# Performance work log

Hardware: AMD Instinct MI355X
Metric: run time of the kernel (lower is better)

The kernel has to match this reference:

```python
import jax, jax.numpy as jnp
import numpy as np

B, L, A, BD, K, M, FP, R, T = 256, 128, 39, 10, 6, 256, 256, 3, 2


def _gru(x, h, w_ih, w_hh, b_ih, b_hh):
    # PyTorch GRUCell: gates ordered (reset, update, new)
    gi = x @ w_ih.T + b_ih
    gh = h @ w_hh.T + b_hh
    i_r, i_z, i_n = jnp.split(gi, 3, axis=-1)
    h_r, h_z, h_n = jnp.split(gh, 3, axis=-1)
    r = jax.nn.sigmoid(i_r + h_r)
    z = jax.nn.sigmoid(i_z + h_z)
    n = jnp.tanh(i_n + r * h_n)
    return (1.0 - z) * n + z * h


def setup_inputs() -> dict:
    key = jax.random.key(0)
    ks = jax.random.split(key, 26)
    n = lambda i, shape: jax.random.normal(ks[i], shape, jnp.float32) * 0.05
    return dict(
        atom_list=jax.random.normal(ks[0], (B, L, A), jnp.float32),
        bond_list=jax.random.normal(ks[1], (B, M, BD), jnp.float32),
        atom_degree_list=jax.random.randint(ks[2], (B, L, K), 0, L),
        bond_degree_list=jax.random.randint(ks[3], (B, L, K), 0, M),
        atom_mask=jnp.ones((B, L), jnp.float32),
        atom_fc_W=n(4, (FP, A)), atom_fc_b=n(5, (FP,)),
        neighbor_fc_W=n(6, (FP, A + BD)), neighbor_fc_b=n(7, (FP,)),
        gru_w_ih=n(8, (R, 3 * FP, FP)), gru_w_hh=n(9, (R, 3 * FP, FP)),
        gru_b_ih=n(10, (R, 3 * FP)), gru_b_hh=n(11, (R, 3 * FP)),
        align_W=n(12, (R, 1, 2 * FP)), align_b=n(13, (R, 1)),
        attend_W=n(14, (R, FP, FP)), attend_b=n(15, (R, FP)),
        mol_gru_w_ih=n(16, (3 * FP, FP)), mol_gru_w_hh=n(17, (3 * FP, FP)),
        mol_gru_b_ih=n(18, (3 * FP,)), mol_gru_b_hh=n(19, (3 * FP,)),
        mol_align_W=n(20, (1, 2 * FP)), mol_align_b=n(21, (1,)),
        mol_attend_W=n(22, (FP, FP)), mol_attend_b=n(23, (FP,)),
    )


def reference(atom_list, bond_list, atom_degree_list, bond_degree_list, atom_mask,
              atom_fc_W, atom_fc_b, neighbor_fc_W, neighbor_fc_b,
              gru_w_ih, gru_w_hh, gru_b_ih, gru_b_hh,
              align_W, align_b, attend_W, attend_b,
              mol_gru_w_ih, mol_gru_w_hh, mol_gru_b_ih, mol_gru_b_hh,
              mol_align_W, mol_align_b, mol_attend_W, mol_attend_b):
    Bn, Ln, _ = atom_list.shape
    Fp = atom_fc_W.shape[0]
    gather = jax.vmap(lambda t, i: t[i])  # per-batch row gather

    atom_pre = atom_list @ atom_fc_W.T + atom_fc_b          # (B,L,FP) pre-relu
    atom_feature = jax.nn.relu(atom_pre)
    afv = [atom_pre]

    bond_neighbor = gather(bond_list, bond_degree_list)      # (B,L,K,BD)
    atom_neighbor = gather(atom_list, atom_degree_list)      # (B,L,K,A)
    nf = jax.nn.relu(jnp.concatenate([atom_neighbor, bond_neighbor], -1)
                     @ neighbor_fc_W.T + neighbor_fc_b)       # (B,L,K,FP)

    pad = atom_degree_list == Ln - 1                          # padding-atom index
    attend_mask = jnp.where(pad, 0.0, 1.0)[..., None]
    softmax_mask = jnp.where(pad, -9.0, 0.0)[..., None]

    h = atom_feature.reshape(Bn * Ln, Fp)
    act = atom_feature
    awv = []
    for d in range(R):
        neigh = nf if d == 0 else gather(act, atom_degree_list)
        fa = jnp.concatenate(
            [jnp.broadcast_to(act[:, :, None, :], neigh.shape), neigh], -1)
        score = jax.nn.relu(fa @ align_W[d].T + align_b[d]) + softmax_mask
        aw = jax.nn.softmax(score, axis=-2) * attend_mask     # (B,L,K,1)
        awv.append(aw)
        ctx = jax.nn.relu(jnp.sum(aw * (neigh @ attend_W[d].T + attend_b[d]), -2))
        h = _gru(ctx.reshape(Bn * Ln, Fp), h,
                 gru_w_ih[d], gru_w_hh[d], gru_b_ih[d], gru_b_hh[d])
        atom_feature = h.reshape(Bn, Ln, Fp)
        act = jax.nn.relu(atom_feature)
        afv.append(act)

    m3 = atom_mask[..., None]
    mol_unb = [jnp.sum(atom_feature * m3, -2)]
    mol_feature = jnp.sum(act * m3, -2)
    act_mol = jax.nn.relu(mol_feature)
    mfv = [mol_feature]
    mawv = []
    mol_smask = jnp.where(m3 == 0, -9e8, 0.0)
    for _ in range(T):
        ma = jnp.concatenate(
            [jnp.broadcast_to(act_mol[:, None, :], act.shape), act], -1)
        ms = jax.nn.relu(ma @ mol_align_W.T + mol_align_b) + mol_smask
        mw = jax.nn.softmax(ms, axis=-2) * m3                 # (B,L,1)
        mawv.append(mw)
        mctx = jax.nn.relu(jnp.sum(mw * (act @ mol_attend_W.T + mol_attend_b), -2))
        mol_feature = _gru(mctx, mol_feature,
                           mol_gru_w_ih, mol_gru_w_hh, mol_gru_b_ih, mol_gru_b_hh)
        mol_unb.append(mol_feature)
        act_mol = jax.nn.relu(mol_feature)
        mfv.append(act_mol)

    return (atom_feature, jnp.stack(afv), jnp.stack(awv), jnp.stack(mfv),
            jnp.stack(mol_unb), jnp.stack(mawv), mol_feature)
```

## Files before the change

kernel.cpp:

```cpp
#include <hip/hip_runtime.h>
#include <hip/hip_bf16.h>

#define BB 256
#define LL 128
#define AA 39
#define BDD 10
#define KK 6
#define MM 256
#define FP 256
#define RR 3
#define TT 2

using short8  = __attribute__((ext_vector_type(8))) short;
using short4v = __attribute__((ext_vector_type(4))) short;
using f32x4   = __attribute__((ext_vector_type(4))) float;
using f32x2   = __attribute__((ext_vector_type(2))) float;

__device__ __forceinline__ short f2bf(float f) {
    union { float f; unsigned u; } v; v.f = f;
    unsigned u = v.u;
    u += 0x7fffu + ((u >> 16) & 1u);
    return (short)(u >> 16);
}
__device__ __forceinline__ float bf2f(short s) {
    union { unsigned u; float f; } v; v.u = ((unsigned)(unsigned short)s) << 16;
    return v.f;
}
__device__ __forceinline__ float wred64(float v) {
#pragma unroll
    for (int off = 32; off >= 1; off >>= 1) v += __shfl_xor(v, off);
    return v;
}

#define GLL(gp, lp) __builtin_amdgcn_global_load_lds( \
    (const __attribute__((address_space(1))) void*)(gp), \
    (__attribute__((address_space(3))) void*)(lp), 16, 0, 0)

__global__ __launch_bounds__(256) void k_transpose(const float* __restrict__ src,
                                                   float* __restrict__ dst, int O, int I) {
    int idx = blockIdx.x * 256 + threadIdx.x;
    if (idx >= O * I) return;
    int o = idx / I, i = idx - o * I;
    dst[i * O + o] = src[idx];
}

__global__ __launch_bounds__(256) void k_prep_gruw(const float* __restrict__ gwih,
                                                   const float* __restrict__ gwhh,
                                                   short* __restrict__ out) {
    int idx = blockIdx.x * 256 + threadIdx.x;
    if (idx >= RR * 2 * 8 * 48 * 512) return;
    int j = idx & 7;
    int lane = (idx >> 3) & 63;
    int blk = idx >> 9;
    int nt = blk % 48;
    int ks = (blk / 48) % 8;
    int mat = (blk / (48 * 8)) % 2;
    int d = blk / (48 * 8 * 2);
    int n = nt * 16 + (lane & 15);
    int k = ks * 32 + (lane >> 4) * 8 + j;
    const float* W = mat ? gwhh : gwih;
    out[idx] = f2bf(W[((size_t)d * 768 + n) * FP + k]);
}

__global__ __launch_bounds__(256) void k_prep_molfrag(const float* __restrict__ mih,
                                                      const float* __restrict__ mhh,
                                                      short* __restrict__ out) {
    int idx = blockIdx.x * 256 + threadIdx.x;
    if (idx >= 2 * 8 * 48 * 512) return;
    int j = idx & 7;
    int lane = (idx >> 3) & 63;
    int blk = idx >> 9;
    int nt = blk % 48;
    int ks = (blk / 48) % 8;
    int mat = blk / (48 * 8);
    int n = nt * 16 + (lane & 15);
    int k = ks * 32 + (lane >> 4) * 8 + j;
    const float* W = mat ? mhh : mih;
    out[idx] = f2bf(W[(size_t)n * FP + k]);
}

__global__ __launch_bounds__(256) void k_prep_waf(const float* __restrict__ atW,
                                                  short* __restrict__ out) {
    int idx = blockIdx.x * 256 + threadIdx.x;
    if (idx >= RR * 8 * 16 * 512) return;
    int j = idx & 7;
    int lane = (idx >> 3) & 63;
    int blk = idx >> 9;
    int nt = blk % 16;
    int ks = (blk / 16) % 8;
    int d = blk / 128;
    int n = nt * 16 + (lane & 15);
    int k = ks * 32 + (lane >> 4) * 8 + j;
    out[idx] = f2bf(atW[(size_t)d * FP * FP + (size_t)n * FP + k]);
}

__global__ __launch_bounds__(256) void k_atom_pre(const float* __restrict__ atom_list,
                                                  const float* __restrict__ WafcT,
                                                  const float* __restrict__ afc_b,
                                                  const float* __restrict__ WnT,
                                                  const float* __restrict__ bn,
                                                  float* __restrict__ out_pre,
                                                  float* __restrict__ hbuf,
                                                  short* __restrict__ hb16,
                                                  short* __restrict__ ApreB) {
    int g0 = blockIdx.x * 8;
    int t = threadIdx.x;
    __shared__ float x[8][AA];
    for (int i = t; i < 8 * AA; i += 256) x[i / AA][i % AA] = atom_list[(size_t)g0 * AA + i];
    __syncthreads();
    float a1[8], a2[8];
    float b1 = afc_b[t], b2 = bn[t];
#pragma unroll
    for (int a = 0; a < 8; ++a) { a1[a] = b1; a2[a] = b2; }
    for (int i = 0; i < AA; ++i) {
        float w1 = WafcT[i * FP + t];
        float w2 = WnT[i * FP + t];
#pragma unroll
        for (int a = 0; a < 8; ++a) { a1[a] += x[a][i] * w1; a2[a] += x[a][i] * w2; }
    }
#pragma unroll
    for (int a = 0; a < 8; ++a) {
        size_t idx = (size_t)(g0 + a) * FP + t;
        out_pre[idx] = a1[a];
        float rl = fmaxf(a1[a], 0.f);
        hbuf[idx] = rl;
        hb16[idx] = f2bf(rl);
        ApreB[idx] = f2bf(a2[a]);
    }
}

__global__ __launch_bounds__(512) void k_awn_d0(
        const short* __restrict__ ACTB,
        const short* __restrict__ SRC,
        const float* __restrict__ bond_list,
        const int* __restrict__ adeg, const int* __restrict__ bdeg,
        const float* __restrict__ WnT,
        const float* __restrict__ alignW, const float* __restrict__ alignBp,
        short* __restrict__ wn_out, float* __restrict__ sw_out,
        float* __restrict__ awv_out) {
    __shared__ short snb[LL * FP];
    const int b = blockIdx.x >> 1;
    const int half = blockIdx.x & 1;
    const int t = threadIdx.x;
    const int wave = t >> 6, lane = t & 63;

    {
        const char* src = (const char*)(SRC + (size_t)b * LL * FP);
#pragma unroll
        for (int it = 0; it < 8; ++it) {
            int off = it * 8192 + wave * 1024 + lane * 16;
            GLL(src + off, (char*)snb + it * 8192 + wave * 1024);
        }
    }

    f32x4 w0 = *(const f32x4*)(alignW + lane * 4);
    f32x4 w1 = *(const f32x4*)(alignW + FP + lane * 4);
    float bias = alignBp[0];

    float wnt[BDD][4];
#pragma unroll
    for (int i = 0; i < BDD; ++i) {
        f32x4 v = *(const f32x4*)(WnT + (AA + i) * FP + lane * 4);
#pragma unroll
        for (int q = 0; q < 4; ++q) wnt[i][q] = v[q];
    }

    __syncthreads();

#pragma unroll
    for (int ai = 0; ai < 8; ++ai) {
        const int al = half * 64 + wave * 8 + ai;
        const int ga = b * LL + al;

        short4v sv = *(const short4v*)(ACTB + (size_t)ga * FP + lane * 4);
        float ss = wred64(bf2f(sv[0]) * w0[0] + bf2f(sv[1]) * w0[1] +
                          bf2f(sv[2]) * w0[2] + bf2f(sv[3]) * w0[3]);

        int jx[KK];
#pragma unroll
        for (int k = 0; k < KK; ++k) jx[k] = adeg[ga * KK + k];

        float nf[KK][4];
        float sc[KK];
#pragma unroll
        for (int k = 0; k < KK; ++k) {
            short4v nv = *(const short4v*)(snb + jx[k] * FP + lane * 4);
            float f0 = bf2f(nv[0]), f1 = bf2f(nv[1]), f2 = bf2f(nv[2]), f3 = bf2f(nv[3]);
            int bi = bdeg[ga * KK + k];
            const float* bp = bond_list + ((size_t)b * MM + bi) * BDD;
            float bb[BDD];
#pragma unroll
            for (int i = 0; i < 5; ++i) {
                f32x2 v2 = *(const f32x2*)(bp + 2 * i);
                bb[2 * i] = v2[0]; bb[2 * i + 1] = v2[1];
            }
            float b0 = 0.f, b1 = 0.f, b2 = 0.f, b3 = 0.f;
#pragma unroll
            for (int i = 0; i < BDD; ++i) {
                b0 += bb[i] * wnt[i][0]; b1 += bb[i] * wnt[i][1];
                b2 += bb[i] * wnt[i][2]; b3 += bb[i] * wnt[i][3];
            }
            f0 = fmaxf(f0 + b0, 0.f); f1 = fmaxf(f1 + b1, 0.f);
            f2 = fmaxf(f2 + b2, 0.f); f3 = fmaxf(f3 + b3, 0.f);
            nf[k][0] = f0; nf[k][1] = f1; nf[k][2] = f2; nf[k][3] = f3;
            float s2 = wred64(f0 * w1[0] + f1 * w1[1] + f2 * w1[2] + f3 * w1[3]);
            float s = fmaxf(ss + s2 + bias, 0.f);
            if (jx[k] == LL - 1) s -= 9.0f;
            sc[k] = s;
        }

        float m = sc[0];
#pragma unroll
        for (int k = 1; k < KK; ++k) m = fmaxf(m, sc[k]);
        float e[KK], den = 0.f;
#pragma unroll
        for (int k = 0; k < KK; ++k) { e[k] = expf(sc[k] - m); den += e[k]; }
        float aw[KK], sumaw = 0.f;
#pragma unroll
        for (int k = 0; k < KK; ++k) {
            aw[k] = (jx[k] == LL - 1) ? 0.f : e[k] / den;
            sumaw += aw[k];
        }
        if (lane < KK) {
            float av = aw[0];
#pragma unroll
            for (int k = 1; k < KK; ++k) if (lane == k) av = aw[k];
            awv_out[(size_t)ga * KK + lane] = av;
        }
        if (lane == 0) sw_out[ga] = sumaw;

        short4v wo;
#pragma unroll
        for (int q = 0; q < 4; ++q) {
            float w = 0.f;
#pragma unroll
            for (int k = 0; k < KK; ++k) w += aw[k] * nf[k][q];
            wo[q] = f2bf(w);
        }
        *(short4v*)(wn_out + (size_t)ga * FP + lane * 4) = wo;
    }
}

__global__ __launch_bounds__(512) void k_ctx_mfma(
        const short* __restrict__ XB,
        const float* __restrict__ SW,
        const short* __restrict__ WaF,
        const float* __restrict__ ab,
        short* __restrict__ ctx_out) {
    __shared__ short lds[2][8192];
    const int t = threadIdx.x;
    const int wave = t >> 6, lane = t & 63;
    const int abase = blockIdx.x * 32 + (wave >> 2) * 16;
    const int wn4 = wave & 3;
    const int lr = lane & 15, lk = lane >> 4;
    const int kofs = blockIdx.x & 7;

#define CSTAGE(i) do { \
        int ke_ = ((i) + kofs) & 7; \
        _Pragma("unroll") \
        for (int e = 0; e < 2; ++e) { \
            int f = wave * 2 + e; \
            GLL(WaF + (size_t)(ke_ * 16 + f) * 512 + lane * 8, &lds[(i) & 1][f * 512]); \
        } } while (0)

    f32x4 acc[4] = {};
    const short8* xrow = (const short8*)(XB + (size_t)(abase + lr) * FP);

    CSTAGE(0);
#pragma unroll
    for (int i = 0; i < 8; ++i) {
        int ke = (i + kofs) & 7;
        short8 ax = xrow[ke * 4 + lk];
        __syncthreads();
        if (i < 7) CSTAGE(i + 1);
#pragma unroll
        for (int sub = 0; sub < 4; ++sub) {
            int nt = wn4 * 4 + sub;
            short8 bf = *(const short8*)(&lds[i & 1][nt * 512 + lane * 8]);
            acc[sub] = __builtin_amdgcn_mfma_f32_16x16x32_bf16(ax, bf, acc[sub], 0, 0, 0);
        }
    }
#undef CSTAGE

#pragma unroll
    for (int sub = 0; sub < 4; ++sub) {
        int c = wn4 * 64 + sub * 16 + lr;
        float abc = ab[c];
#pragma unroll
        for (int q = 0; q < 4; ++q) {
            int atom = abase + lk * 4 + q;
            float v = acc[sub][q] + SW[atom] * abc;
            ctx_out[(size_t)atom * FP + c] = f2bf(fmaxf(v, 0.f));
        }
    }
}

__global__ __launch_bounds__(512) void k_actx(int d,
        const short* __restrict__ ACTB,
        const int* __restrict__ adeg,
        const float* __restrict__ alW, const float* __restrict__ alb,
        const short* __restrict__ WaF, const float* __restrict__ atb,
        short* __restrict__ ctx_out, float* __restrict__ awv_out) {
    __shared__ __align__(16) short aS[32768];
    __shared__ __align__(16) short cS[32768];
    __shared__ int   jxS[LL * KK];
    __shared__ float awS[LL * KK];
    __shared__ float swS[LL];

    const int b = blockIdx.x;
    const int t = threadIdx.x;
    const int wave = t >> 6, lane = t & 63;
    const int lr = lane & 15, lk = lane >> 4;

#define SLAB_OFF(r, cb) ((((r) * 512 + (cb))) ^ ((((r) & 7)) << 4))
#define A4R(r, c)  (*(const short4v*)((const char*)aS + SLAB_OFF(r, (c) * 2)))
#define C8R(r, c)  (*(const short8*)((const char*)cS + SLAB_OFF(r, (c) * 2)))
#define CW4(r, c, v) (*(short4v*)((char*)cS + SLAB_OFF(r, (c) * 2)) = (v))

    {
        const char* src = (const char*)(ACTB + (size_t)b * LL * FP);
#pragma unroll
        for (int it = 0; it < 8; ++it) {
            int off = it * 8192 + wave * 1024 + lane * 16;
            int so = off ^ (((off >> 9) & 7) << 4);
            GLL(src + so, (char*)aS + off);
        }
        for (int i = t; i < LL * KK; i += 512) jxS[i] = adeg[b * LL * KK + i];
    }
    __syncthreads();

    {
        f32x4 w0 = *(const f32x4*)(alW + (size_t)d * 2 * FP + lane * 4);
        f32x4 w1 = *(const f32x4*)(alW + (size_t)d * 2 * FP + FP + lane * 4);
        float bias = alb[d];
        for (int ai = 0; ai < 16; ++ai) {
            int a = wave * 16 + ai;
            short4v sv = A4R(a, lane * 4);
            float ss = wred64(bf2f(sv[0]) * w0[0] + bf2f(sv[1]) * w0[1] +
                              bf2f(sv[2]) * w0[2] + bf2f(sv[3]) * w0[3]);
            float sc[KK]; int jx[KK];
#pragma unroll
            for (int k = 0; k < KK; ++k) {
                int j = jxS[a * KK + k]; jx[k] = j;
                short4v nv = A4R(j, lane * 4);
                float s2 = wred64(bf2f(nv[0]) * w1[0] + bf2f(nv[1]) * w1[1] +
                                  bf2f(nv[2]) * w1[2] + bf2f(nv[3]) * w1[3]);
                float s = fmaxf(ss + s2 + bias, 0.f);
                if (j == LL - 1) s -= 9.0f;
                sc[k] = s;
            }
            float m = sc[0];
#pragma unroll
            for (int k = 1; k < KK; ++k) m = fmaxf(m, sc[k]);
            float e[KK], den = 0.f;
#pragma unroll
            for (int k = 0; k < KK; ++k) { e[k] = expf(sc[k] - m); den += e[k]; }
            float aw[KK], sumaw = 0.f;
#pragma unroll
            for (int k = 0; k < KK; ++k) {
                aw[k] = (jx[k] == LL - 1) ? 0.f : e[k] / den;
                sumaw += aw[k];
            }
            if (lane < KK) {
                float av = aw[0];
#pragma unroll
                for (int k = 1; k < KK; ++k) if (lane == k) av = aw[k];
                awS[a * KK + lane] = av;
                awv_out[((size_t)b * LL + a) * KK + lane] = av;
            }
            if (lane == 0) swS[a] = sumaw;
        }
    }
    __syncthreads();

    for (int ai = 0; ai < 16; ++ai) {
        int a = wave * 16 + ai;
        float a0 = 0.f, a1 = 0.f, a2 = 0.f, a3 = 0.f;
#pragma unroll
        for (int k = 0; k < KK; ++k) {
            float awv = awS[a * KK + k];
            short4v nv = A4R(jxS[a * KK + k], lane * 4);
            a0 += awv * bf2f(nv[0]);
            a1 += awv * bf2f(nv[1]);
            a2 += awv * bf2f(nv[2]);
            a3 += awv * bf2f(nv[3]);
        }
        short4v wo; wo[0] = f2bf(a0); wo[1] = f2bf(a1); wo[2] = f2bf(a2); wo[3] = f2bf(a3);
        CW4(a, lane * 4, wo);
    }
    __syncthreads();

    {
        const int rg = wave >> 1, csl = wave & 1;
        f32x4 acc[2][8] = {};
        const short8* wb = (const short8*)(WaF + (size_t)d * 8 * 16 * 512);
        for (int ks = 0; ks < 8; ++ks) {
            short8 a0 = C8R(rg * 32 + lr, ks * 32 + lk * 8);
            short8 a1 = C8R(rg * 32 + 16 + lr, ks * 32 + lk * 8);
#pragma unroll
            for (int nt2 = 0; nt2 < 8; ++nt2) {
                short8 bf = wb[(size_t)(ks * 16 + csl * 8 + nt2) * 64 + lane];
                acc[0][nt2] = __builtin_amdgcn_mfma_f32_16x16x32_bf16(a0, bf, acc[0][nt2], 0, 0, 0);
                acc[1][nt2] = __builtin_amdgcn_mfma_f32_16x16x32_bf16(a1, bf, acc[1][nt2], 0, 0, 0);
            }
        }
#pragma unroll
        for (int rt = 0; rt < 2; ++rt)
#pragma unroll
        for (int nt2 = 0; nt2 < 8; ++nt2) {
            int col = csl * 128 + nt2 * 16 + lr;
            float abv = atb[d * FP + col];
#pragma unroll
            for (int q = 0; q < 4; ++q) {
                int row = rg * 32 + rt * 16 + lk * 4 + q;
                float v = acc[rt][nt2][q] + swS[row] * abv;
                ctx_out[((size_t)b * LL + row) * FP + col] = f2bf(fmaxf(v, 0.f));
            }
        }
    }
#undef SLAB_OFF
#undef A4R
#undef C8R
#undef CW4
}

template<int LAST>
__global__ __launch_bounds__(512) void k_gru_mfma(
        const short* __restrict__ XB,
        const short* __restrict__ HBl,
        float* __restrict__ hbuf,
        const short* __restrict__ Bih,
        const short* __restrict__ Bhh,
        const float* __restrict__ bih, const float* __restrict__ bhh,
        float* __restrict__ act_out,
        short* __restrict__ HB_out,
        short* __restrict__ ACT_out) {
    __shared__ short ldsB[3][12288];
    __shared__ short ldsA[2][16384];
    const int t = threadIdx.x;
    const int wave = t >> 6, lane = t & 63;
    const int rh = wave >> 2;
    const int wn = wave & 3;
    const int lr = lane & 15, lk = lane >> 4;
    const int bid = blockIdx.x;
    const int kofs = bid & 7;
    const int abase = bid * 64;

#define PKS(p)  ((((p) >> 2) + kofs) & 7)
#define STAGEP(p) do { \
        const short* base_ = ((((p) >> 1) & 1) ? Bhh : Bih) + (size_t)PKS(p) * 24576; \
        const int h_ = (p) & 1; \
        _Pragma("unroll") \
        for (int e = 0; e < 3; ++e) { \
            int j = wave * 3 + e; \
            int nt = 4 * (j >> 1) + 2 * h_ + (j & 1); \
            GLL(base_ + nt * 512 + lane * 8, &ldsB[(p) % 3][j * 512]); \
        } } while (0)
#define LDA_READ(s, r, c) (*(const short8*)((const char*)ldsA[s] + \
        ((((r) * 512 + (c) * 2)) ^ ((((r) & 7)) << 4))))
#define LDA_READ1(s, r, c) (*(const short*)((const char*)ldsA[s] + \
        ((((r) * 512 + (c) * 2)) ^ ((((r) & 7)) << 4))))

    {
        const char* xsrc = (const char*)(XB + (size_t)abase * FP);
        const char* hsrc = (const char*)(HBl + (size_t)abase * FP);
#pragma unroll
        for (int it = 0; it < 4; ++it) {
            int off = it * 8192 + wave * 1024 + lane * 16;
            int src = off ^ (((off >> 9) & 7) << 4);
            GLL(xsrc + src, (char*)ldsA[0] + off);
            GLL(hsrc + src, (char*)ldsA[1] + off);
        }
    }
    STAGEP(0);
    STAGEP(1);

    f32x4 acc_rz[2][8] = {};
    f32x4 acc_in[2][4] = {};
    f32x4 acc_hn[2][4] = {};

    short8 ax0{}, ah0{}, ax1{}, ah1{};
#pragma unroll
    for (int p = 0; p < 32; ++p) {
        if (p < 31) { asm volatile("s_waitcnt vmcnt(3)" ::: "memory"); }
        else        { asm volatile("s_waitcnt vmcnt(0)" ::: "memory"); }
        __builtin_amdgcn_s_barrier();
        __builtin_amdgcn_sched_barrier(0);
        if (p < 30) STAGEP(p + 2);
        const int h_ = p & 1;
        const int mat = (p >> 1) & 1;
        if ((p & 3) == 0) {
            int ks = PKS(p);
            int c = ks * 32 + lk * 8;
            ax0 = LDA_READ(0, rh * 32 + lr, c);
            ah0 = LDA_READ(1, rh * 32 + lr, c);
            ax1 = LDA_READ(0, rh * 32 + 16 + lr, c);
            ah1 = LDA_READ(1, rh * 32 + 16 + lr, c);
        }
#pragma unroll
        for (int rg = 0; rg < 2; ++rg) {
            const short8 a8 = mat ? (rg ? ah1 : ah0) : (rg ? ax1 : ax0);
#pragma unroll
            for (int g = 0; g < 3; ++g) {
#pragma unroll
                for (int s2 = 0; s2 < 2; ++s2) {
                    const int sub = 2 * h_ + s2;
                    const int j = ((4 * g + wn) << 1) | s2;
                    short8 bf = *(const short8*)(&ldsB[p % 3][j * 512 + lane * 8]);
                    if (g < 2)
                        acc_rz[rg][g * 4 + sub] = __builtin_amdgcn_mfma_f32_16x16x32_bf16(a8, bf, acc_rz[rg][g * 4 + sub], 0, 0, 0);
                    else if (mat)
                        acc_hn[rg][sub] = __builtin_amdgcn_mfma_f32_16x16x32_bf16(a8, bf, acc_hn[rg][sub], 0, 0, 0);
                    else
                        acc_in[rg][sub] = __builtin_amdgcn_mfma_f32_16x16x32_bf16(a8, bf, acc_in[rg][sub], 0, 0, 0);
                }
            }
        }
    }
#undef STAGEP
#undef PKS

#pragma unroll
    for (int sub = 0; sub < 4; ++sub) {
        int c = wn * 64 + sub * 16 + lr;
        float brz_r = bih[c] + bhh[c];
        float brz_z = bih[FP + c] + bhh[FP + c];
        float bin_ = bih[2 * FP + c];
        float bhn = bhh[2 * FP + c];
#pragma unroll
        for (int rg = 0; rg < 2; ++rg) {
#pragma unroll
            for (int q = 0; q < 4; ++q) {
                int row = rh * 32 + rg * 16 + lk * 4 + q;
                int atom = abase + row;
                size_t idx = (size_t)atom * FP + c;
                float hold = bf2f(LDA_READ1(1, row, c));
                float r = 1.f / (1.f + expf(-(acc_rz[rg][0 * 4 + sub][q] + brz_r)));
                float z = 1.f / (1.f + expf(-(acc_rz[rg][1 * 4 + sub][q] + brz_z)));
                float n = tanhf(acc_in[rg][sub][q] + bin_ + r * (acc_hn[rg][sub][q] + bhn));
                float hn = (1.f - z) * n + z * hold;
                float rl = fmaxf(hn, 0.f);
                act_out[idx] = rl;
                if constexpr (LAST) {
                    hbuf[idx] = hn;
                } else {
                    HB_out[idx] = f2bf(hn);
                    ACT_out[idx] = f2bf(rl);
                }
            }
        }
    }
#undef LDA_READ
#undef LDA_READ1
}

__global__ __launch_bounds__(256) void k_mol_reduce(const float* __restrict__ hbuf,
                                                    const float* __restrict__ act,
                                                    const float* __restrict__ mask,
                                                    const float* __restrict__ malW,
                                                    float* __restrict__ o_unb0,
                                                    float* __restrict__ o_mfv0,
                                                    float* __restrict__ molF,
                                                    short* __restrict__ MOLFb,
                                                    float* __restrict__ S2g) {
    int b = blockIdx.x, t = threadIdx.x;
    int wave = t >> 6, lane = t & 63;
    float s1 = 0.f, s2 = 0.f;
    for (int l = 0; l < LL; ++l) {
        float mk = mask[b * LL + l];
        s1 += hbuf[((size_t)b * LL + l) * FP + t] * mk;
        s2 += act[((size_t)b * LL + l) * FP + t] * mk;
    }
    o_unb0[b * FP + t] = s1;
    o_mfv0[b * FP + t] = s2;
    molF[b * FP + t] = s2;
    MOLFb[b * FP + t] = f2bf(s2);

    for (int l = wave; l < LL; l += 4) {
        float v2 = 0.f;
#pragma unroll
        for (int q = 0; q < 4; ++q) {
            int i = lane + 64 * q;
            v2 += act[((size_t)b * LL + l) * FP + i] * malW[FP + i];
        }
        v2 = wred64(v2);
        if (lane == 0) S2g[b * LL + l] = v2;
    }
}

__global__ __launch_bounds__(256) void k_mstep(int step,
        const float* __restrict__ act,
        const float* __restrict__ molF,
        const float* __restrict__ mask,
        const float* __restrict__ S2g,
        const float* __restrict__ malW, const float* __restrict__ malb,
        const float* __restrict__ MWaT, const float* __restrict__ matb,
        short* __restrict__ MCTXb,
        float* __restrict__ o_mawv) {
    int b = blockIdx.x, t = threadIdx.x;
    int wave = t >> 6, lane = t & 63;
    __shared__ float sS[LL], mwS[LL], waS[FP];
    __shared__ float red[4];

    float hprev = molF[b * FP + t];
    float am = fmaxf(hprev, 0.f);

    float v = am * malW[t];
    v = wred64(v);
    if (lane == 0) red[wave] = v;
    __syncthreads();
    float s_self = red[0] + red[1] + red[2] + red[3];

    if (t < LL) {
        float s = fmaxf(s_self + S2g[b * LL + t] + malb[0], 0.f);
        if (mask[b * LL + t] == 0.f) s += -9e8f;
        sS[t] = s;
    }
    __syncthreads();

    float m = -1e30f;
    for (int l = 0; l < LL; ++l) m = fmaxf(m, sS[l]);
    float den = 0.f;
    for (int l = 0; l < LL; ++l) den += expf(sS[l] - m);
    if (t < LL) {
        float w = expf(sS[t] - m) / den * mask[b * LL + t];
        mwS[t] = w;
        o_mawv[(size_t)step * (BB * LL) + b * LL + t] = w;
    }
    __syncthreads();

    float sumaw = 0.f;
    for (int l = 0; l < LL; ++l) sumaw += mwS[l];

    float wa = 0.f;
    for (int l = 0; l < LL; ++l) wa += mwS[l] * act[((size_t)b * LL + l) * FP + t];
    waS[t] = wa;
    __syncthreads();

    float acc = sumaw * matb[t];
    for (int i = 0; i < FP; ++i) acc += waS[i] * MWaT[i * FP + t];
    MCTXb[b * FP + t] = f2bf(fmaxf(acc, 0.f));
}

__global__ __launch_bounds__(512) void k_mol_gru(int step,
        const short* __restrict__ XB,
        const short* __restrict__ HBl,
        const short* __restrict__ Bih,
        const short* __restrict__ Bhh,
        const float* __restrict__ bih, const float* __restrict__ bhh,
        float* __restrict__ o_unb, float* __restrict__ o_mfv,
        float* __restrict__ molF, short* __restrict__ MOLFb,
        float* __restrict__ o_molfeat) {
    __shared__ short ldsB[3][12288];
    __shared__ short ldsA[2][16384];
    const int t = threadIdx.x;
    const int wave = t >> 6, lane = t & 63;
    const int rh = wave >> 2;
    const int wn = wave & 3;
    const int lr = lane & 15, lk = lane >> 4;
    const int bid = blockIdx.x;
    const int kofs = bid & 7;
    const int abase = bid * 64;

#define PKS(p)  ((((p) >> 2) + kofs) & 7)
#define STAGEP(p) do { \
        const short* base_ = ((((p) >> 1) & 1) ? Bhh : Bih) + (size_t)PKS(p) * 24576; \
        const int h_ = (p) & 1; \
        _Pragma("unroll") \
        for (int e = 0; e < 3; ++e) { \
            int j = wave * 3 + e; \
            int nt = 4 * (j >> 1) + 2 * h_ + (j & 1); \
            GLL(base_ + nt * 512 + lane * 8, &ldsB[(p) % 3][j * 512]); \
        } } while (0)
#define LDA_READ(s, r, c) (*(const short8*)((const char*)ldsA[s] + \
        ((((r) * 512 + (c) * 2)) ^ ((((r) & 7)) << 4))))
#define LDA_READ1(s, r, c) (*(const short*)((const char*)ldsA[s] + \
        ((((r) * 512 + (c) * 2)) ^ ((((r) & 7)) << 4))))

    {
        const char* xsrc = (const char*)(XB + (size_t)abase * FP);
        const char* hsrc = (const char*)(HBl + (size_t)abase * FP);
#pragma unroll
        for (int it = 0; it < 4; ++it) {
            int off = it * 8192 + wave * 1024 + lane * 16;
            int src = off ^ (((off >> 9) & 7) << 4);
            GLL(xsrc + src, (char*)ldsA[0] + off);
            GLL(hsrc + src, (char*)ldsA[1] + off);
        }
    }
    STAGEP(0);
    STAGEP(1);

    f32x4 acc_rz[2][8] = {};
    f32x4 acc_in[2][4] = {};
    f32x4 acc_hn[2][4] = {};

    short8 ax0{}, ah0{}, ax1{}, ah1{};
#pragma unroll
    for (int p = 0; p < 32; ++p) {
        if (p < 31) { asm volatile("s_waitcnt vmcnt(3)" ::: "memory"); }
        else        { asm volatile("s_waitcnt vmcnt(0)" ::: "memory"); }
        __builtin_amdgcn_s_barrier();
        __builtin_amdgcn_sched_barrier(0);
        if (p < 30) STAGEP(p + 2);
        const int h_ = p & 1;
        const int mat = (p >> 1) & 1;
        if ((p & 3) == 0) {
            int ks = PKS(p);
            int c = ks * 32 + lk * 8;
            ax0 = LDA_READ(0, rh * 32 + lr, c);
            ah0 = LDA_READ(1, rh * 32 + lr, c);
            ax1 = LDA_READ(0, rh * 32 + 16 + lr, c);
            ah1 = LDA_READ(1, rh * 32 + 16 + lr, c);
        }
#pragma unroll
        for (int rg = 0; rg < 2; ++rg) {
            const short8 a8 = mat ? (rg ? ah1 : ah0) : (rg ? ax1 : ax0);
#pragma unroll
            for (int g = 0; g < 3; ++g) {
#pragma unroll
                for (int s2 = 0; s2 < 2; ++s2) {
                    const int sub = 2 * h_ + s2;
                    const int j = ((4 * g + wn) << 1) | s2;
                    short8 bf = *(const short8*)(&ldsB[p % 3][j * 512 + lane * 8]);
                    if (g < 2)
                        acc_rz[rg][g * 4 + sub] = __builtin_amdgcn_mfma_f32_16x16x32_bf16(a8, bf, acc_rz[rg][g * 4 + sub], 0, 0, 0);
                    else if (mat)
                        acc_hn[rg][sub] = __builtin_amdgcn_mfma_f32_16x16x32_bf16(a8, bf, acc_hn[rg][sub], 0, 0, 0);
                    else
                        acc_in[rg][sub] = __builtin_amdgcn_mfma_f32_16x16x32_bf16(a8, bf, acc_in[rg][sub], 0, 0, 0);
                }
            }
        }
    }
#undef STAGEP
#undef PKS

#pragma unroll
    for (int sub = 0; sub < 4; ++sub) {
        int c = wn * 64 + sub * 16 + lr;
        float brz_r = bih[c] + bhh[c];
        float brz_z = bih[FP + c] + bhh[FP + c];
        float bin_ = bih[2 * FP + c];
        float bhn = bhh[2 * FP + c];
#pragma unroll
        for (int rg = 0; rg < 2; ++rg) {
#pragma unroll
            for (int q = 0; q < 4; ++q) {
                int row = rh * 32 + rg * 16 + lk * 4 + q;
                int m = abase + row;
                size_t idx = (size_t)m * FP + c;
                float hold = bf2f(LDA_READ1(1, row, c));
                float r = 1.f / (1.f + expf(-(acc_rz[rg][0 * 4 + sub][q] + brz_r)));
                float z = 1.f / (1.f + expf(-(acc_rz[rg][1 * 4 + sub][q] + brz_z)));
                float n = tanhf(acc_in[rg][sub][q] + bin_ + r * (acc_hn[rg][sub][q] + bhn));
                float hn = (1.f - z) * n + z * hold;
                o_unb[(size_t)(step + 1) * (BB * FP) + idx] = hn;
                o_mfv[(size_t)(step + 1) * (BB * FP) + idx] = fmaxf(hn, 0.f);
                molF[idx] = hn;
                MOLFb[idx] = f2bf(hn);
                if (step == TT - 1) o_molfeat[idx] = hn;
            }
        }
    }
#undef LDA_READ
#undef LDA_READ1
}

extern "C" void kernel_launch(void* const* d_in, const int* in_sizes, int n_in,
                              void* d_out, int out_size, void* d_ws, size_t ws_size,
                              hipStream_t stream) {
    const float* atom_list = (const float*)d_in[0];
    const float* bond_list = (const float*)d_in[1];
    const int*   adeg      = (const int*)d_in[2];
    const int*   bdeg      = (const int*)d_in[3];
    const float* amask     = (const float*)d_in[4];
    const float* atom_fc_W = (const float*)d_in[5];
    const float* atom_fc_b = (const float*)d_in[6];
    const float* nfc_W     = (const float*)d_in[7];
    const float* nfc_b     = (const float*)d_in[8];
    const float* gwih      = (const float*)d_in[9];
    const float* gwhh      = (const float*)d_in[10];
    const float* gbih      = (const float*)d_in[11];
    const float* gbhh      = (const float*)d_in[12];
    const float* alW       = (const float*)d_in[13];
    const float* alb       = (const float*)d_in[14];
    const float* atW       = (const float*)d_in[15];
    const float* atb       = (const float*)d_in[16];
    const float* mgwih     = (const float*)d_in[17];
    const float* mgwhh     = (const float*)d_in[18];
    const float* mgbih     = (const float*)d_in[19];
    const float* mgbhh     = (const float*)d_in[20];
    const float* malW      = (const float*)d_in[21];
    const float* malb      = (const float*)d_in[22];
    const float* matW      = (const float*)d_in[23];
    const float* matb      = (const float*)d_in[24];

    const size_t BLF = (size_t)BB * LL * FP;
    float* out = (float*)d_out;
    float* O0 = out;
    float* O1 = out + BLF;
    float* O2 = O1 + 4 * BLF;
    float* O3 = O2 + (size_t)RR * BB * LL * KK;
    float* O4 = O3 + (size_t)(TT + 1) * BB * FP;
    float* O5 = O4 + (size_t)(TT + 1) * BB * FP;
    float* O6 = O5 + (size_t)TT * BB * LL;

    float* ws = (float*)d_ws;
    short* XB   = (short*)ws;
    short* XB2  = XB + BLF;
    short* HBb  = XB + 2 * BLF;
    short* ACTB = XB + 3 * BLF;
    float* rest = ws + 2 * BLF;
    short* ApreB = (short*)rest;
    float* SW    = rest + BLF / 2;
    float* MOLF  = SW + (size_t)BB * LL;
    float* WafcT = MOLF + (size_t)BB * FP;
    float* WnT   = WafcT + AA * FP;
    float* MWaT  = WnT + (AA + BDD) * FP;
    short* MolGW = (short*)(MWaT + (size_t)FP * FP);
    short* GW    = MolGW + (size_t)2 * 8 * 48 * 512;
    short* WaF   = GW + (size_t)RR * 2 * 8 * 48 * 512;
    short* MCTXb = WaF + (size_t)RR * 8 * 16 * 512;
    short* MOLFb = MCTXb + (size_t)BB * FP;
    float* S2g   = (float*)(MOLFb + (size_t)BB * FP);
    (void)ws_size; (void)in_sizes; (void)n_in; (void)out_size;

    auto tr = [&](const float* src, float* dst, int O, int I) {
        int n = O * I;
        k_transpose<<<(n + 255) / 256, 256, 0, stream>>>(src, dst, O, I);
    };
    tr(atom_fc_W, WafcT, FP, AA);
    tr(nfc_W, WnT, FP, AA + BDD);
    tr(matW, MWaT, FP, FP);

    {
        int n = RR * 2 * 8 * 48 * 512;
        k_prep_gruw<<<(n + 255) / 256, 256, 0, stream>>>(gwih, gwhh, GW);
        int n2 = RR * 8 * 16 * 512;
        k_prep_waf<<<(n2 + 255) / 256, 256, 0, stream>>>(atW, WaF);
        int n3 = 2 * 8 * 48 * 512;
        k_prep_molfrag<<<(n3 + 255) / 256, 256, 0, stream>>>(mgwih, mgwhh, MolGW);
    }

    k_atom_pre<<<BB * LL / 8, 256, 0, stream>>>(atom_list, WafcT, atom_fc_b,
                                                WnT, nfc_b, O1, O0, HBb, ApreB);

    const size_t wblk = (size_t)8 * 48 * 512;
    for (int d = 0; d < RR; ++d) {
        if (d == 0) {
            k_awn_d0<<<BB * 2, 512, 0, stream>>>(HBb, ApreB, bond_list, adeg, bdeg,
                    WnT, alW, alb, XB, SW, O2);
            k_ctx_mfma<<<BB * LL / 32, 512, 0, stream>>>(XB, SW, WaF,
                    atb, XB2);
        } else {
            k_actx<<<BB, 512, 0, stream>>>(d, ACTB, adeg,
                    alW, alb, WaF, atb,
                    XB2, O2 + (size_t)d * BB * LL * KK);
        }
        if (d == RR - 1) {
            k_gru_mfma<1><<<BB * LL / 64, 512, 0, stream>>>(XB2, HBb, O0,
                    GW + (size_t)(d * 2 + 0) * wblk, GW + (size_t)(d * 2 + 1) * wblk,
                    gbih + (size_t)d * 768, gbhh + (size_t)d * 768,
                    O1 + (size_t)(d + 1) * BLF, HBb, ACTB);
        } else {
            k_gru_mfma<0><<<BB * LL / 64, 512, 0, stream>>>(XB2, HBb, O0,
                    GW + (size_t)(d * 2 + 0) * wblk, GW + (size_t)(d * 2 + 1) * wblk,
                    gbih + (size_t)d * 768, gbhh + (size_t)d * 768,
                    O1 + (size_t)(d + 1) * BLF, HBb, ACTB);
        }
    }

    const float* actFin = O1 + (size_t)RR * BLF;
    k_mol_reduce<<<BB, 256, 0, stream>>>(O0, actFin, amask, malW,
                                         O4, O3, MOLF, MOLFb, S2g);
    for (int st = 0; st < TT; ++st) {
        k_mstep<<<BB, 256, 0, stream>>>(st, actFin, MOLF, amask, S2g,
                malW, malb, MWaT, matb, MCTXb, O5);
        k_mol_gru<<<4, 512, 0, stream>>>(st, MCTXb, MOLFb,
                MolGW, MolGW + wblk, mgbih, mgbhh,
                O4, O3, MOLF, MOLFb, O6);
    }
}
```

Before: 569.6 us.

## Fuse depth-0 neighbor attention and context matmul into one per-molecule kernel

Merges the depth-0 neighbor-weighting kernel and the separate context MFMA kernel into one kernel that runs one block per molecule. The weighted neighbor features and softmax sums stay in swizzled LDS and feed the MFMA directly, so the global round trip of the intermediate and one launch are gone. Degree indices are staged in LDS. The fp32 relu copy from the atom pre-pass is also no longer written. The trade-off is half as many blocks and heavier per-block LDS use, which lowers parallelism.

```diff
diff --git a/kernel.cpp b/kernel.cpp
--- a/kernel.cpp
+++ b/kernel.cpp
@@ -100,7 +100,6 @@
                                                   const float* __restrict__ WnT,
                                                   const float* __restrict__ bn,
                                                   float* __restrict__ out_pre,
-                                                  float* __restrict__ hbuf,
                                                   short* __restrict__ hb16,
                                                   short* __restrict__ ApreB) {
     int g0 = blockIdx.x * 8;
@@ -122,40 +121,53 @@
     for (int a = 0; a < 8; ++a) {
         size_t idx = (size_t)(g0 + a) * FP + t;
         out_pre[idx] = a1[a];
-        float rl = fmaxf(a1[a], 0.f);
-        hbuf[idx] = rl;
-        hb16[idx] = f2bf(rl);
+        hb16[idx] = f2bf(fmaxf(a1[a], 0.f));
         ApreB[idx] = f2bf(a2[a]);
     }
 }
 
-__global__ __launch_bounds__(512) void k_awn_d0(
+__global__ __launch_bounds__(512) void k_actx_d0(
         const short* __restrict__ ACTB,
-        const short* __restrict__ SRC,
+        const short* __restrict__ ApreB,
         const float* __restrict__ bond_list,
         const int* __restrict__ adeg, const int* __restrict__ bdeg,
         const float* __restrict__ WnT,
-        const float* __restrict__ alignW, const float* __restrict__ alignBp,
-        short* __restrict__ wn_out, float* __restrict__ sw_out,
-        float* __restrict__ awv_out) {
-    __shared__ short snb[LL * FP];
-    const int b = blockIdx.x >> 1;
-    const int half = blockIdx.x & 1;
+        const float* __restrict__ alW, const float* __restrict__ alb,
+        const short* __restrict__ WaF, const float* __restrict__ atb,
+        short* __restrict__ ctx_out, float* __restrict__ awv_out) {
+    __shared__ __align__(16) short aS[32768];
+    __shared__ __align__(16) short cS[32768];
+    __shared__ int jxS[LL * KK];
+    __shared__ int bxS[LL * KK];
+    __shared__ float swS[LL];
+
+    const int b = blockIdx.x;
     const int t = threadIdx.x;
     const int wave = t >> 6, lane = t & 63;
+    const int lr = lane & 15, lk = lane >> 4;
+
+#define SLAB_OFF(r, cb) ((((r) * 512 + (cb))) ^ ((((r) & 7)) << 4))
+#define A4R(r, c)  (*(const short4v*)((const char*)aS + SLAB_OFF(r, (c) * 2)))
+#define C8R(r, c)  (*(const short8*)((const char*)cS + SLAB_OFF(r, (c) * 2)))
+#define CW4(r, c, v) (*(short4v*)((char*)cS + SLAB_OFF(r, (c) * 2)) = (v))
 
     {
-        const char* src = (const char*)(SRC + (size_t)b * LL * FP);
+        const char* src = (const char*)(ApreB + (size_t)b * LL * FP);
 #pragma unroll
         for (int it = 0; it < 8; ++it) {
             int off = it * 8192 + wave * 1024 + lane * 16;
-            GLL(src + off, (char*)snb + it * 8192 + wave * 1024);
-        }
-    }
-
-    f32x4 w0 = *(const f32x4*)(alignW + lane * 4);
-    f32x4 w1 = *(const f32x4*)(alignW + FP + lane * 4);
-    float bias = alignBp[0];
+            int so = off ^ (((off >> 9) & 7) << 4);
+            GLL(src + so, (char*)aS + off);
+        }
+        for (int i = t; i < LL * KK; i += 512) {
+            jxS[i] = adeg[b * LL * KK + i];
+            bxS[i] = bdeg[b * LL * KK + i];
+        }
+    }
+
+    f32x4 w0 = *(const f32x4*)(alW + lane * 4);
+    f32x4 w1 = *(const f32x4*)(alW + FP + lane * 4);
+    float bias = alb[0];
 
     float wnt[BDD][4];
 #pragma unroll
@@ -164,13 +176,11 @@
 #pragma unroll
         for (int q = 0; q < 4; ++q) wnt[i][q] = v[q];
     }
-
-    __syncthreads();
-
-#pragma unroll
-    for (int ai = 0; ai < 8; ++ai) {
-        const int al = half * 64 + wave * 8 + ai;
-        const int ga = b * LL + al;
+    __syncthreads();
+
+    for (int ai = 0; ai < 16; ++ai) {
+        const int a = wave * 16 + ai;
+        const int ga = b * LL + a;
 
         short4v sv = *(const short4v*)(ACTB + (size_t)ga * FP + lane * 4);
         float ss = wred64(bf2f(sv[0]) * w0[0] + bf2f(sv[1]) * w0[1] +
@@ -178,15 +188,15 @@
 
         int jx[KK];
 #pragma unroll
-        for (int k = 0; k < KK; ++k) jx[k] = adeg[ga * KK + k];
+        for (int k = 0; k < KK; ++k) jx[k] = jxS[a * KK + k];
 
         float nf[KK][4];
         float sc[KK];
 #pragma unroll
         for (int k = 0; k < KK; ++k) {
-            short4v nv = *(const short4v*)(snb + jx[k] * FP + lane * 4);
+            short4v nv = A4R(jx[k], lane * 4);
             float f0 = bf2f(nv[0]), f1 = bf2f(nv[1]), f2 = bf2f(nv[2]), f3 = bf2f(nv[3]);
-            int bi = bdeg[ga * KK + k];
+            int bi = bxS[a * KK + k];
             const float* bp = bond_list + ((size_t)b * MM + bi) * BDD;
             float bb[BDD];
 #pragma unroll
@@ -227,7 +237,7 @@
             for (int k = 1; k < KK; ++k) if (lane == k) av = aw[k];
             awv_out[(size_t)ga * KK + lane] = av;
         }
-        if (lane == 0) sw_out[ga] = sumaw;
+        if (lane == 0) swS[a] = sumaw;
 
         short4v wo;
 #pragma unroll
@@ -237,62 +247,42 @@
             for (int k = 0; k < KK; ++k) w += aw[k] * nf[k][q];
             wo[q] = f2bf(w);
         }
-        *(short4v*)(wn_out + (size_t)ga * FP + lane * 4) = wo;
-    }
-}
-
-__global__ __launch_bounds__(512) void k_ctx_mfma(
-        const short* __restrict__ XB,
-        const float* __restrict__ SW,
-        const short* __restrict__ WaF,
-        const float* __restrict__ ab,
-        short* __restrict__ ctx_out) {
-    __shared__ short lds[2][8192];
-    const int t = threadIdx.x;
-    const int wave = t >> 6, lane = t & 63;
-    const int abase = blockIdx.x * 32 + (wave >> 2) * 16;
-    const int wn4 = wave & 3;
-    const int lr = lane & 15, lk = lane >> 4;
-    const int kofs = blockIdx.x & 7;
-
-#define CSTAGE(i) do { \
-        int ke_ = ((i) + kofs) & 7; \
-        _Pragma("unroll") \
-        for (int e = 0; e < 2; ++e) { \
-            int f = wave * 2 + e; \
-            GLL(WaF + (size_t)(ke_ * 16 + f) * 512 + lane * 8, &lds[(i) & 1][f * 512]); \
-        } } while (0)
-
-    f32x4 acc[4] = {};
-    const short8* xrow = (const short8*)(XB + (size_t)(abase + lr) * FP);
-
-    CSTAGE(0);
-#pragma unroll
-    for (int i = 0; i < 8; ++i) {
-        int ke = (i + kofs) & 7;
-        short8 ax = xrow[ke * 4 + lk];
-        __syncthreads();
-        if (i < 7) CSTAGE(i + 1);
-#pragma unroll
-        for (int sub = 0; sub < 4; ++sub) {
-            int nt = wn4 * 4 + sub;
-            short8 bf = *(const short8*)(&lds[i & 1][nt * 512 + lane * 8]);
-            acc[sub] = __builtin_amdgcn_mfma_f32_16x16x32_bf16(ax, bf, acc[sub], 0, 0, 0);
-        }
-    }
-#undef CSTAGE
-
-#pragma unroll
-    for (int sub = 0; sub < 4; ++sub) {
-        int c = wn4 * 64 + sub * 16 + lr;
-        float abc = ab[c];
-#pragma unroll
-        for (int q = 0; q < 4; ++q) {
-            int atom = abase + lk * 4 + q;
-            float v = acc[sub][q] + SW[atom] * abc;
-            ctx_out[(size_t)atom * FP + c] = f2bf(fmaxf(v, 0.f));
-        }
-    }
+        CW4(a, lane * 4, wo);
+    }
+    __syncthreads();
+
+    {
+        const int rg = wave >> 1, csl = wave & 1;
+        f32x4 acc[2][8] = {};
+        const short8* wb = (const short8*)WaF;
+        for (int ks = 0; ks < 8; ++ks) {
+            short8 a0 = C8R(rg * 32 + lr, ks * 32 + lk * 8);
+            short8 a1 = C8R(rg * 32 + 16 + lr, ks * 32 + lk * 8);
+#pragma unroll
+            for (int nt2 = 0; nt2 < 8; ++nt2) {
+                short8 bf = wb[(size_t)(ks * 16 + csl * 8 + nt2) * 64 + lane];
+                acc[0][nt2] = __builtin_amdgcn_mfma_f32_16x16x32_bf16(a0, bf, acc[0][nt2], 0, 0, 0);
+                acc[1][nt2] = __builtin_amdgcn_mfma_f32_16x16x32_bf16(a1, bf, acc[1][nt2], 0, 0, 0);
+            }
+        }
+#pragma unroll
+        for (int rt = 0; rt < 2; ++rt)
+#pragma unroll
+        for (int nt2 = 0; nt2 < 8; ++nt2) {
+            int col = csl * 128 + nt2 * 16 + lr;
+            float abv = atb[col];
+#pragma unroll
+            for (int q = 0; q < 4; ++q) {
+                int row = rg * 32 + rt * 16 + lk * 4 + q;
+                float v = acc[rt][nt2][q] + swS[row] * abv;
+                ctx_out[((size_t)b * LL + row) * FP + col] = f2bf(fmaxf(v, 0.f));
+            }
+        }
+    }
+#undef SLAB_OFF
+#undef A4R
+#undef C8R
+#undef CW4
 }
 
 __global__ __launch_bounds__(512) void k_actx(int d,
@@ -844,15 +834,13 @@
     }
 
     k_atom_pre<<<BB * LL / 8, 256, 0, stream>>>(atom_list, WafcT, atom_fc_b,
-                                                WnT, nfc_b, O1, O0, HBb, ApreB);
+                                                WnT, nfc_b, O1, HBb, ApreB);
 
     const size_t wblk = (size_t)8 * 48 * 512;
     for (int d = 0; d < RR; ++d) {
         if (d == 0) {
-            k_awn_d0<<<BB * 2, 512, 0, stream>>>(HBb, ApreB, bond_list, adeg, bdeg,
-                    WnT, alW, alb, XB, SW, O2);
-            k_ctx_mfma<<<BB * LL / 32, 512, 0, stream>>>(XB, SW, WaF,
-                    atb, XB2);
+            k_actx_d0<<<BB, 512, 0, stream>>>(HBb, ApreB, bond_list, adeg, bdeg,
+                    WnT, alW, alb, WaF, atb, XB2, O2);
         } else {
             k_actx<<<BB, 512, 0, stream>>>(d, ACTB, adeg,
                     alW, alb, WaF, atb,
```

Result: faster. 541.2 us (-5.0%).
